# Kernel tuning notes

Measured on AMD Instinct MI355X. Metric: run time of the kernel, lower is better.

Reference implementation:

```python
import jax, jax.numpy as jnp
import numpy as np

E, H, I, T, K = 32, 1024, 768, 2048, 8


def setup_inputs() -> dict:
    key = jax.random.key(0)
    ks = jax.random.split(key, 6)
    hidden_states = jax.random.normal(ks[0], (T, H), dtype=jnp.float32)
    routing_weights = jax.random.uniform(ks[1], (T, K), dtype=jnp.float32)
    selected_experts = jax.random.randint(ks[2], (T, K), 0, E, dtype=jnp.int32)
    scale = 0.02
    gate_proj = jax.random.normal(ks[3], (E, I, H), dtype=jnp.float32) * scale
    up_proj = jax.random.normal(ks[4], (E, I, H), dtype=jnp.float32) * scale
    down_proj = jax.random.normal(ks[5], (E, H, I), dtype=jnp.float32) * scale
    return {
        "hidden_states": hidden_states,
        "routing_weights": routing_weights,
        "selected_experts": selected_experts,
        "gate_proj": gate_proj,
        "up_proj": up_proj,
        "down_proj": down_proj,
    }


def reference(hidden_states, routing_weights, selected_experts, gate_proj, up_proj, down_proj):
    # hidden_states: [T, H]; routing_weights/selected_experts: [T, K]
    # gate/up: [E, I, H]; down: [E, H, I]
    T_, _ = hidden_states.shape
    E_ = gate_proj.shape[0]
    # combine[t, e] = sum_k routing_weights[t, k] * 1[selected_experts[t, k] == e]
    combine = jnp.zeros((T_, E_), hidden_states.dtype).at[
        jnp.arange(T_)[:, None], selected_experts
    ].add(routing_weights)
    g = jnp.einsum('th,eih->eti', hidden_states, gate_proj)   # [E, T, I]
    u = jnp.einsum('th,eih->eti', hidden_states, up_proj)     # [E, T, I]
    h = jax.nn.silu(g) * u                                    # SwiGLU
    d = jnp.einsum('eti,ehi->eth', h, down_proj)              # [E, T, H]
    out = jnp.einsum('eth,te->th', d, combine)                # weighted combine
    return out
```

## Files before the change

kernel.cpp:

```cpp
#include <hip/hip_runtime.h>
#include <hip/hip_bf16.h>
#include <math.h>

#define E_N 32
#define H_N 1024
#define I_N 768
#define T_N 2048
#define K_N 8
#define MT  128
#define NPAIRS (T_N * K_N)
#define MAX_SLOTS (NPAIRS + E_N * MT)
#define MAX_TILES (NPAIRS / MT + E_N)
#define RS 40

typedef __attribute__((ext_vector_type(8))) short bf16x8;
typedef __attribute__((ext_vector_type(4))) short bf16x4;
typedef __attribute__((ext_vector_type(8))) float f32x8;
typedef __attribute__((ext_vector_type(4))) float f32x4;

__device__ __forceinline__ unsigned pk2(float a, float b) {
    unsigned ua = __float_as_uint(a) + 0x8000u;
    unsigned ub = __float_as_uint(b) + 0x8000u;
    return (ua >> 16) | (ub & 0xffff0000u);
}
__device__ __forceinline__ bf16x8 cvt8(f32x8 v) {
    union { unsigned u[4]; bf16x8 h; } r;
    r.u[0] = pk2(v[0], v[1]); r.u[1] = pk2(v[2], v[3]);
    r.u[2] = pk2(v[4], v[5]); r.u[3] = pk2(v[6], v[7]);
    return r.h;
}
__device__ __forceinline__ float bf2f(short s) {
    return __uint_as_float(((unsigned)(unsigned short)s) << 16);
}

__global__ void route_kernel(const int* __restrict__ sel,
                             int* __restrict__ slot_token,
                             int* __restrict__ pair_slot,
                             int* __restrict__ tile_expert,
                             int* __restrict__ tile_row0,
                             int* __restrict__ n_tiles_out) {
    __shared__ int cnt[E_N], off[E_N], cur[E_N];
    int tid = threadIdx.x;
    if (tid < E_N) cnt[tid] = 0;
    __syncthreads();
    for (int p = tid; p < NPAIRS; p += blockDim.x)
        atomicAdd(&cnt[sel[p]], 1);
    __syncthreads();
    if (tid == 0) {
        int acc = 0, tt = 0;
        for (int e = 0; e < E_N; ++e) {
            off[e] = acc;
            cur[e] = 0;
            int nt = (cnt[e] + MT - 1) / MT;
            for (int i = 0; i < nt; ++i) {
                tile_expert[tt] = e;
                tile_row0[tt] = acc + i * MT;
                ++tt;
            }
            acc += nt * MT;
        }
        *n_tiles_out = tt;
    }
    __syncthreads();
    for (int p = tid; p < NPAIRS; p += blockDim.x) {
        int e = sel[p];
        int slot = off[e] + atomicAdd(&cur[e], 1);
        slot_token[slot] = p / K_N;
        pair_slot[p] = slot;
    }
}

__global__ __launch_bounds__(256) void gather_kernel(
    const float* __restrict__ hs,
    const int* __restrict__ slot_token,
    short* __restrict__ x_buf) {
    int idx = blockIdx.x * 256 + threadIdx.x;
    int slot = idx >> 8;
    int pos = (idx & 255) * 4;
    int tok = slot_token[slot];
    union { unsigned u[2]; bf16x4 s; } o;
    if (tok >= 0) {
        f32x4 v = *(const f32x4*)(hs + (size_t)tok * H_N + pos);
        o.u[0] = pk2(v[0], v[1]);
        o.u[1] = pk2(v[2], v[3]);
    } else {
        o.u[0] = 0; o.u[1] = 0;
    }
    *(bf16x4*)(x_buf + (size_t)slot * H_N + pos) = o.s;
}

__global__ __launch_bounds__(256, 2) void gateup_kernel(
    const short* __restrict__ x_buf,
    const float* __restrict__ gate,
    const float* __restrict__ up,
    const int* __restrict__ tile_expert,
    const int* __restrict__ tile_row0,
    const int* __restrict__ n_tiles,
    __hip_bfloat16* __restrict__ h_buf) {
    int id = blockIdx.x;
    int W = (id & 7) * 120 + (id >> 3);
    int tile = W % MAX_TILES;
    int ycol = W / MAX_TILES;
    if (tile >= *n_tiles) return;
    __shared__ short sA[128 * RS];
    __shared__ short sG[128 * RS];
    __shared__ short sU[128 * RS];
    int e = tile_expert[tile];
    int row0 = tile_row0[tile];
    int col0 = ycol * 128;
    int tid = threadIdx.x;
    int wave = tid >> 6, lane = tid & 63, quad = lane >> 4, r16 = lane & 15;
    int m0w = (wave >> 1) * 64, n0w = (wave & 1) * 64;
    int srow = tid >> 2;
    int scol = (tid & 3) * 8;

    f32x4 accG[4][4], accU[4][4];
#pragma unroll
    for (int i = 0; i < 4; ++i)
#pragma unroll
        for (int j = 0; j < 4; ++j) {
            accG[i][j] = (f32x4){0.f, 0.f, 0.f, 0.f};
            accU[i][j] = (f32x4){0.f, 0.f, 0.f, 0.f};
        }

    const size_t gbase = ((size_t)e * I_N + col0) * H_N;

    bf16x8 pa[2];
    f32x8 pg[2], pu[2];
#pragma unroll
    for (int r = 0; r < 2; ++r) {
        int row = r * 64 + srow;
        pa[r] = *(const bf16x8*)(x_buf + (size_t)(row0 + row) * H_N + scol);
        pg[r] = *(const f32x8*)(gate + gbase + (size_t)row * H_N + scol);
        pu[r] = *(const f32x8*)(up + gbase + (size_t)row * H_N + scol);
    }

#pragma unroll 1
    for (int k0 = 0; k0 < H_N; k0 += 32) {
        __syncthreads();
#pragma unroll
        for (int r = 0; r < 2; ++r) {
            int row = r * 64 + srow;
            *(bf16x8*)&sA[row * RS + scol] = pa[r];
            *(bf16x8*)&sG[row * RS + scol] = cvt8(pg[r]);
            *(bf16x8*)&sU[row * RS + scol] = cvt8(pu[r]);
        }
        __syncthreads();
        if (k0 + 32 < H_N) {
            int kn = k0 + 32;
#pragma unroll
            for (int r = 0; r < 2; ++r) {
                int row = r * 64 + srow;
                pa[r] = *(const bf16x8*)(x_buf + (size_t)(row0 + row) * H_N + kn + scol);
                pg[r] = *(const f32x8*)(gate + gbase + (size_t)row * H_N + kn + scol);
                pu[r] = *(const f32x8*)(up + gbase + (size_t)row * H_N + kn + scol);
            }
        }
        bf16x8 af[4], bg[4], bu[4];
#pragma unroll
        for (int mi = 0; mi < 4; ++mi)
            af[mi] = *(const bf16x8*)&sA[(m0w + mi * 16 + r16) * RS + quad * 8];
#pragma unroll
        for (int ni = 0; ni < 4; ++ni) {
            bg[ni] = *(const bf16x8*)&sG[(n0w + ni * 16 + r16) * RS + quad * 8];
            bu[ni] = *(const bf16x8*)&sU[(n0w + ni * 16 + r16) * RS + quad * 8];
        }
#pragma unroll
        for (int mi = 0; mi < 4; ++mi)
#pragma unroll
            for (int ni = 0; ni < 4; ++ni) {
                accG[mi][ni] = __builtin_amdgcn_mfma_f32_16x16x32_bf16(af[mi], bg[ni], accG[mi][ni], 0, 0, 0);
                accU[mi][ni] = __builtin_amdgcn_mfma_f32_16x16x32_bf16(af[mi], bu[ni], accU[mi][ni], 0, 0, 0);
            }
    }
#pragma unroll
    for (int mi = 0; mi < 4; ++mi)
#pragma unroll
        for (int ni = 0; ni < 4; ++ni)
#pragma unroll
            for (int r = 0; r < 4; ++r) {
                int m = m0w + mi * 16 + quad * 4 + r;
                int n = col0 + n0w + ni * 16 + r16;
                float g = accG[mi][ni][r], u = accU[mi][ni][r];
                float hval = g * u / (1.0f + __expf(-g));
                h_buf[(size_t)(row0 + m) * I_N + n] = __float2bfloat16(hval);
            }
}

__global__ __launch_bounds__(256, 2) void down_kernel(
    const __hip_bfloat16* __restrict__ h_buf,
    const float* __restrict__ down,
    const int* __restrict__ tile_expert,
    const int* __restrict__ tile_row0,
    const int* __restrict__ n_tiles,
    short* __restrict__ d_buf) {
    int id = blockIdx.x;
    int W = (id & 7) * 160 + (id >> 3);
    int tile = W % MAX_TILES;
    int ycol = W / MAX_TILES;
    if (tile >= *n_tiles) return;
    __shared__ short sA[128 * RS];
    __shared__ short sB[128 * RS];
    int e = tile_expert[tile];
    int row0 = tile_row0[tile];
    int col0 = ycol * 128;
    int tid = threadIdx.x;
    int wave = tid >> 6, lane = tid & 63, quad = lane >> 4, r16 = lane & 15;
    int m0w = (wave >> 1) * 64, n0w = (wave & 1) * 64;
    int srow = tid >> 2;
    int scol = (tid & 3) * 8;

    f32x4 acc[4][4];
#pragma unroll
    for (int i = 0; i < 4; ++i)
#pragma unroll
        for (int j = 0; j < 4; ++j) acc[i][j] = (f32x4){0.f, 0.f, 0.f, 0.f};

    const short* hb = (const short*)h_buf;
    const size_t dbase = ((size_t)e * H_N + col0) * I_N;

    bf16x8 pa[2];
    f32x8 pb[2];
#pragma unroll
    for (int r = 0; r < 2; ++r) {
        int row = r * 64 + srow;
        pa[r] = *(const bf16x8*)(hb + (size_t)(row0 + row) * I_N + scol);
        pb[r] = *(const f32x8*)(down + dbase + (size_t)row * I_N + scol);
    }

#pragma unroll 1
    for (int k0 = 0; k0 < I_N; k0 += 32) {
        __syncthreads();
#pragma unroll
        for (int r = 0; r < 2; ++r) {
            int row = r * 64 + srow;
            *(bf16x8*)&sA[row * RS + scol] = pa[r];
            *(bf16x8*)&sB[row * RS + scol] = cvt8(pb[r]);
        }
        __syncthreads();
        if (k0 + 32 < I_N) {
            int kn = k0 + 32;
#pragma unroll
            for (int r = 0; r < 2; ++r) {
                int row = r * 64 + srow;
                pa[r] = *(const bf16x8*)(hb + (size_t)(row0 + row) * I_N + kn + scol);
                pb[r] = *(const f32x8*)(down + dbase + (size_t)row * I_N + kn + scol);
            }
        }
        bf16x8 af[4], bf[4];
#pragma unroll
        for (int mi = 0; mi < 4; ++mi)
            af[mi] = *(const bf16x8*)&sA[(m0w + mi * 16 + r16) * RS + quad * 8];
#pragma unroll
        for (int ni = 0; ni < 4; ++ni)
            bf[ni] = *(const bf16x8*)&sB[(n0w + ni * 16 + r16) * RS + quad * 8];
#pragma unroll
        for (int mi = 0; mi < 4; ++mi)
#pragma unroll
            for (int ni = 0; ni < 4; ++ni)
                acc[mi][ni] = __builtin_amdgcn_mfma_f32_16x16x32_bf16(af[mi], bf[ni], acc[mi][ni], 0, 0, 0);
    }
#pragma unroll
    for (int mi = 0; mi < 4; ++mi)
#pragma unroll
        for (int ni = 0; ni < 4; ++ni)
#pragma unroll
            for (int r = 0; r < 4; ++r) {
                int m = m0w + mi * 16 + quad * 4 + r;
                int n = col0 + n0w + ni * 16 + r16;
                unsigned u = __float_as_uint(acc[mi][ni][r]) + 0x8000u;
                d_buf[(size_t)(row0 + m) * H_N + n] = (short)(u >> 16);
            }
}

__global__ __launch_bounds__(256) void combine_kernel(
    const short* __restrict__ d_buf,
    const int* __restrict__ pair_slot,
    const float* __restrict__ rw,
    float* __restrict__ out) {
    int idx = blockIdx.x * blockDim.x + threadIdx.x;
    int t = idx >> 10;
    int h = idx & (H_N - 1);
    float acc = 0.f;
#pragma unroll
    for (int k = 0; k < K_N; ++k) {
        int slot = pair_slot[t * K_N + k];
        float w = rw[t * K_N + k];
        acc += w * bf2f(d_buf[(size_t)slot * H_N + h]);
    }
    out[idx] = acc;
}

extern "C" void kernel_launch(void* const* d_in, const int* in_sizes, int n_in,
                              void* d_out, int out_size, void* d_ws, size_t ws_size,
                              hipStream_t stream) {
    const float* hs   = (const float*)d_in[0];
    const float* rw   = (const float*)d_in[1];
    const int*   sel  = (const int*)d_in[2];
    const float* gate = (const float*)d_in[3];
    const float* up   = (const float*)d_in[4];
    const float* down = (const float*)d_in[5];
    float* out = (float*)d_out;

    char* ws = (char*)d_ws;
    int* slot_token  = (int*)ws;  ws += ((size_t)MAX_SLOTS * 4 + 255) / 256 * 256;
    int* pair_slot   = (int*)ws;  ws += ((size_t)NPAIRS * 4 + 255) / 256 * 256;
    int* tile_expert = (int*)ws;  ws += ((size_t)MAX_TILES * 4 + 255) / 256 * 256;
    int* tile_row0   = (int*)ws;  ws += ((size_t)MAX_TILES * 4 + 255) / 256 * 256;
    int* n_tiles     = (int*)ws;  ws += 256;
    short* x_buf = (short*)ws;    ws += ((size_t)MAX_SLOTS * H_N * 2 + 255) / 256 * 256;
    __hip_bfloat16* h_buf = (__hip_bfloat16*)ws;
    short* d_buf = x_buf;

    hipMemsetAsync(slot_token, 0xFF, (size_t)MAX_SLOTS * 4, stream);
    route_kernel<<<1, 256, 0, stream>>>(sel, slot_token, pair_slot,
                                        tile_expert, tile_row0, n_tiles);
    gather_kernel<<<(MAX_SLOTS * H_N / 4) / 256, 256, 0, stream>>>(hs, slot_token, x_buf);

    gateup_kernel<<<MAX_TILES * (I_N / 128), 256, 0, stream>>>(
        x_buf, gate, up, tile_expert, tile_row0, n_tiles, h_buf);

    down_kernel<<<MAX_TILES * (H_N / 128), 256, 0, stream>>>(
        h_buf, down, tile_expert, tile_row0, n_tiles, d_buf);

    combine_kernel<<<(T_N * H_N) / 256, 256, 0, stream>>>(d_buf, pair_slot,
                                                          rw, out);
}
```

Baseline: 490.3 us.

## Double-buffer LDS tiles in gate/up and down GEMMs with one barrier per step

Both grouped GEMM kernels now keep two LDS buffers. Each iteration reads fragments from the current buffer, writes the prefetched next tile into the other buffer, issues global loads two steps ahead, and ends with a single barrier instead of two. MFMA blocks are wrapped in s_setprio, and the LDS row stride changes from 40 to 36 shorts to alter bank mapping. This doubles LDS use, which may limit occupancy. The new padding may also misalign the 16-byte vector LDS accesses or raise bank conflicts.

Measured after the change: 486.5 us. No clear change (-0.8%).

```diff
diff --git a/kernel.cpp b/kernel.cpp
--- a/kernel.cpp
+++ b/kernel.cpp
@@ -11,7 +11,7 @@
 #define NPAIRS (T_N * K_N)
 #define MAX_SLOTS (NPAIRS + E_N * MT)
 #define MAX_TILES (NPAIRS / MT + E_N)
-#define RS 40
+#define RS 36
 
 typedef __attribute__((ext_vector_type(8))) short bf16x8;
 typedef __attribute__((ext_vector_type(4))) short bf16x4;
@@ -31,6 +31,11 @@
 }
 __device__ __forceinline__ float bf2f(short s) {
     return __uint_as_float(((unsigned)(unsigned short)s) << 16);
+}
+
+__device__ __forceinline__ void lds_barrier() {
+    asm volatile("s_waitcnt lgkmcnt(0)" ::: "memory");
+    __builtin_amdgcn_s_barrier();
 }
 
 __global__ void route_kernel(const int* __restrict__ sel,
@@ -102,9 +107,9 @@
     int tile = W % MAX_TILES;
     int ycol = W / MAX_TILES;
     if (tile >= *n_tiles) return;
-    __shared__ short sA[128 * RS];
-    __shared__ short sG[128 * RS];
-    __shared__ short sU[128 * RS];
+    __shared__ short sA[2][128 * RS];
+    __shared__ short sG[2][128 * RS];
+    __shared__ short sU[2][128 * RS];
     int e = tile_expert[tile];
     int row0 = tile_row0[tile];
     int col0 = ycol * 128;
@@ -124,47 +129,66 @@
         }
 
     const size_t gbase = ((size_t)e * I_N + col0) * H_N;
+    const short* xrow = x_buf + (size_t)row0 * H_N;
 
     bf16x8 pa[2];
     f32x8 pg[2], pu[2];
 #pragma unroll
     for (int r = 0; r < 2; ++r) {
         int row = r * 64 + srow;
-        pa[r] = *(const bf16x8*)(x_buf + (size_t)(row0 + row) * H_N + scol);
+        pa[r] = *(const bf16x8*)(xrow + (size_t)row * H_N + scol);
         pg[r] = *(const f32x8*)(gate + gbase + (size_t)row * H_N + scol);
         pu[r] = *(const f32x8*)(up + gbase + (size_t)row * H_N + scol);
     }
-
+#pragma unroll
+    for (int r = 0; r < 2; ++r) {
+        int row = r * 64 + srow;
+        *(bf16x8*)&sA[0][row * RS + scol] = pa[r];
+        *(bf16x8*)&sG[0][row * RS + scol] = cvt8(pg[r]);
+        *(bf16x8*)&sU[0][row * RS + scol] = cvt8(pu[r]);
+    }
+#pragma unroll
+    for (int r = 0; r < 2; ++r) {
+        int row = r * 64 + srow;
+        pa[r] = *(const bf16x8*)(xrow + (size_t)row * H_N + 32 + scol);
+        pg[r] = *(const f32x8*)(gate + gbase + (size_t)row * H_N + 32 + scol);
+        pu[r] = *(const f32x8*)(up + gbase + (size_t)row * H_N + 32 + scol);
+    }
+    lds_barrier();
+
+    int cur = 0;
 #pragma unroll 1
     for (int k0 = 0; k0 < H_N; k0 += 32) {
-        __syncthreads();
-#pragma unroll
-        for (int r = 0; r < 2; ++r) {
-            int row = r * 64 + srow;
-            *(bf16x8*)&sA[row * RS + scol] = pa[r];
-            *(bf16x8*)&sG[row * RS + scol] = cvt8(pg[r]);
-            *(bf16x8*)&sU[row * RS + scol] = cvt8(pu[r]);
-        }
-        __syncthreads();
+        bf16x8 af[4], bg[4], bu[4];
+#pragma unroll
+        for (int mi = 0; mi < 4; ++mi)
+            af[mi] = *(const bf16x8*)&sA[cur][(m0w + mi * 16 + r16) * RS + quad * 8];
+#pragma unroll
+        for (int ni = 0; ni < 4; ++ni) {
+            bg[ni] = *(const bf16x8*)&sG[cur][(n0w + ni * 16 + r16) * RS + quad * 8];
+            bu[ni] = *(const bf16x8*)&sU[cur][(n0w + ni * 16 + r16) * RS + quad * 8];
+        }
         if (k0 + 32 < H_N) {
-            int kn = k0 + 32;
+            int nxt = cur ^ 1;
 #pragma unroll
             for (int r = 0; r < 2; ++r) {
                 int row = r * 64 + srow;
-                pa[r] = *(const bf16x8*)(x_buf + (size_t)(row0 + row) * H_N + kn + scol);
-                pg[r] = *(const f32x8*)(gate + gbase + (size_t)row * H_N + kn + scol);
-                pu[r] = *(const f32x8*)(up + gbase + (size_t)row * H_N + kn + scol);
-            }
-        }
-        bf16x8 af[4], bg[4], bu[4];
-#pragma unroll
-        for (int mi = 0; mi < 4; ++mi)
-            af[mi] = *(const bf16x8*)&sA[(m0w + mi * 16 + r16) * RS + quad * 8];
-#pragma unroll
-        for (int ni = 0; ni < 4; ++ni) {
-            bg[ni] = *(const bf16x8*)&sG[(n0w + ni * 16 + r16) * RS + quad * 8];
-            bu[ni] = *(const bf16x8*)&sU[(n0w + ni * 16 + r16) * RS + quad * 8];
-        }
+                *(bf16x8*)&sA[nxt][row * RS + scol] = pa[r];
+                *(bf16x8*)&sG[nxt][row * RS + scol] = cvt8(pg[r]);
+                *(bf16x8*)&sU[nxt][row * RS + scol] = cvt8(pu[r]);
+            }
+            if (k0 + 64 < H_N) {
+                int kn = k0 + 64;
+#pragma unroll
+                for (int r = 0; r < 2; ++r) {
+                    int row = r * 64 + srow;
+                    pa[r] = *(const bf16x8*)(xrow + (size_t)row * H_N + kn + scol);
+                    pg[r] = *(const f32x8*)(gate + gbase + (size_t)row * H_N + kn + scol);
+                    pu[r] = *(const f32x8*)(up + gbase + (size_t)row * H_N + kn + scol);
+                }
+            }
+        }
+        __builtin_amdgcn_s_setprio(1);
 #pragma unroll
         for (int mi = 0; mi < 4; ++mi)
 #pragma unroll
@@ -172,6 +196,9 @@
                 accG[mi][ni] = __builtin_amdgcn_mfma_f32_16x16x32_bf16(af[mi], bg[ni], accG[mi][ni], 0, 0, 0);
                 accU[mi][ni] = __builtin_amdgcn_mfma_f32_16x16x32_bf16(af[mi], bu[ni], accU[mi][ni], 0, 0, 0);
             }
+        __builtin_amdgcn_s_setprio(0);
+        if (k0 + 32 < H_N) lds_barrier();
+        cur ^= 1;
     }
 #pragma unroll
     for (int mi = 0; mi < 4; ++mi)
@@ -199,8 +226,8 @@
     int tile = W % MAX_TILES;
     int ycol = W / MAX_TILES;
     if (tile >= *n_tiles) return;
-    __shared__ short sA[128 * RS];
-    __shared__ short sB[128 * RS];
+    __shared__ short sA[2][128 * RS];
+    __shared__ short sB[2][128 * RS];
     int e = tile_expert[tile];
     int row0 = tile_row0[tile];
     int col0 = ycol * 128;
@@ -218,47 +245,67 @@
 
     const short* hb = (const short*)h_buf;
     const size_t dbase = ((size_t)e * H_N + col0) * I_N;
+    const short* hrow = hb + (size_t)row0 * I_N;
 
     bf16x8 pa[2];
     f32x8 pb[2];
 #pragma unroll
     for (int r = 0; r < 2; ++r) {
         int row = r * 64 + srow;
-        pa[r] = *(const bf16x8*)(hb + (size_t)(row0 + row) * I_N + scol);
+        pa[r] = *(const bf16x8*)(hrow + (size_t)row * I_N + scol);
         pb[r] = *(const f32x8*)(down + dbase + (size_t)row * I_N + scol);
     }
-
+#pragma unroll
+    for (int r = 0; r < 2; ++r) {
+        int row = r * 64 + srow;
+        *(bf16x8*)&sA[0][row * RS + scol] = pa[r];
+        *(bf16x8*)&sB[0][row * RS + scol] = cvt8(pb[r]);
+    }
+#pragma unroll
+    for (int r = 0; r < 2; ++r) {
+        int row = r * 64 + srow;
+        pa[r] = *(const bf16x8*)(hrow + (size_t)row * I_N + 32 + scol);
+        pb[r] = *(const f32x8*)(down + dbase + (size_t)row * I_N + 32 + scol);
+    }
+    lds_barrier();
+
+    int cur = 0;
 #pragma unroll 1
     for (int k0 = 0; k0 < I_N; k0 += 32) {
-        __syncthreads();
-#pragma unroll
-        for (int r = 0; r < 2; ++r) {
-            int row = r * 64 + srow;
-            *(bf16x8*)&sA[row * RS + scol] = pa[r];
-            *(bf16x8*)&sB[row * RS + scol] = cvt8(pb[r]);
-        }
-        __syncthreads();
+        bf16x8 af[4], bf[4];
+#pragma unroll
+        for (int mi = 0; mi < 4; ++mi)
+            af[mi] = *(const bf16x8*)&sA[cur][(m0w + mi * 16 + r16) * RS + quad * 8];
+#pragma unroll
+        for (int ni = 0; ni < 4; ++ni)
+            bf[ni] = *(const bf16x8*)&sB[cur][(n0w + ni * 16 + r16) * RS + quad * 8];
         if (k0 + 32 < I_N) {
-            int kn = k0 + 32;
+            int nxt = cur ^ 1;
 #pragma unroll
             for (int r = 0; r < 2; ++r) {
                 int row = r * 64 + srow;
-                pa[r] = *(const bf16x8*)(hb + (size_t)(row0 + row) * I_N + kn + scol);
-                pb[r] = *(const f32x8*)(down + dbase + (size_t)row * I_N + kn + scol);
-            }
-        }
-        bf16x8 af[4], bf[4];
-#pragma unroll
-        for (int mi = 0; mi < 4; ++mi)
-            af[mi] = *(const bf16x8*)&sA[(m0w + mi * 16 + r16) * RS + quad * 8];
-#pragma unroll
-        for (int ni = 0; ni < 4; ++ni)
-            bf[ni] = *(const bf16x8*)&sB[(n0w + ni * 16 + r16) * RS + quad * 8];
+                *(bf16x8*)&sA[nxt][row * RS + scol] = pa[r];
+                *(bf16x8*)&sB[nxt][row * RS + scol] = cvt8(pb[r]);
+            }
+            if (k0 + 64 < I_N) {
+                int kn = k0 + 64;
+#pragma unroll
+                for (int r = 0; r < 2; ++r) {
+                    int row = r * 64 + srow;
+                    pa[r] = *(const bf16x8*)(hrow + (size_t)row * I_N + kn + scol);
+                    pb[r] = *(const f32x8*)(down + dbase + (size_t)row * I_N + kn + scol);
+                }
+            }
+        }
+        __builtin_amdgcn_s_setprio(1);
 #pragma unroll
         for (int mi = 0; mi < 4; ++mi)
 #pragma unroll
             for (int ni = 0; ni < 4; ++ni)
                 acc[mi][ni] = __builtin_amdgcn_mfma_f32_16x16x32_bf16(af[mi], bf[ni], acc[mi][ni], 0, 0, 0);
+        __builtin_amdgcn_s_setprio(0);
+        if (k0 + 32 < I_N) lds_barrier();
+        cur ^= 1;
     }
 #pragma unroll
     for (int mi = 0; mi < 4; ++mi)
```

## Pre-convert expert weights to bf16 and stage tiles via direct global-to-LDS loads

Applied to the files above, without the earlier changes.

Adds a conversion pass that writes the gate, up and down weights to bf16 in workspace, so the GEMM kernels read half as many bytes per tile and skip the per-tile fp32-to-bf16 conversion. The GEMM tile loads now use global_load_lds to write straight into unpadded LDS, replacing the register prefetch double-buffer. MFMA sections are wrapped in s_setprio, and down_kernel's launch bound rises to 3 blocks. The trade-offs: the weights are fully read and rewritten on every call, the overlap from register prefetch is lost, and the unpadded LDS layout may cause bank conflicts.

Result: slower. 524.2 us (+6.9%).

```diff
diff --git a/kernel.cpp b/kernel.cpp
--- a/kernel.cpp
+++ b/kernel.cpp
@@ -11,7 +11,6 @@
 #define NPAIRS (T_N * K_N)
 #define MAX_SLOTS (NPAIRS + E_N * MT)
 #define MAX_TILES (NPAIRS / MT + E_N)
-#define RS 40
 
 typedef __attribute__((ext_vector_type(8))) short bf16x8;
 typedef __attribute__((ext_vector_type(4))) short bf16x4;
@@ -31,6 +30,12 @@
 }
 __device__ __forceinline__ float bf2f(short s) {
     return __uint_as_float(((unsigned)(unsigned short)s) << 16);
+}
+
+__device__ __forceinline__ void gload16(const void* g, void* l) {
+    __builtin_amdgcn_global_load_lds(
+        (const __attribute__((address_space(1))) unsigned int*)g,
+        (__attribute__((address_space(3))) unsigned int*)l, 16, 0, 0);
 }
 
 __global__ void route_kernel(const int* __restrict__ sel,
@@ -89,10 +94,20 @@
     *(bf16x4*)(x_buf + (size_t)slot * H_N + pos) = o.s;
 }
 
+__global__ __launch_bounds__(256) void cvt_kernel(
+    const float* __restrict__ src, short* __restrict__ dst, int n8) {
+    int i = blockIdx.x * 256 + threadIdx.x;
+    int stride = gridDim.x * 256;
+    for (; i < n8; i += stride) {
+        f32x8 v = *(const f32x8*)(src + (size_t)i * 8);
+        *(bf16x8*)(dst + (size_t)i * 8) = cvt8(v);
+    }
+}
+
 __global__ __launch_bounds__(256, 2) void gateup_kernel(
     const short* __restrict__ x_buf,
-    const float* __restrict__ gate,
-    const float* __restrict__ up,
+    const short* __restrict__ wg,
+    const short* __restrict__ wu,
     const int* __restrict__ tile_expert,
     const int* __restrict__ tile_row0,
     const int* __restrict__ n_tiles,
@@ -102,17 +117,17 @@
     int tile = W % MAX_TILES;
     int ycol = W / MAX_TILES;
     if (tile >= *n_tiles) return;
-    __shared__ short sA[128 * RS];
-    __shared__ short sG[128 * RS];
-    __shared__ short sU[128 * RS];
+    __shared__ short sA[128 * 32];
+    __shared__ short sG[128 * 32];
+    __shared__ short sU[128 * 32];
     int e = tile_expert[tile];
     int row0 = tile_row0[tile];
     int col0 = ycol * 128;
     int tid = threadIdx.x;
     int wave = tid >> 6, lane = tid & 63, quad = lane >> 4, r16 = lane & 15;
     int m0w = (wave >> 1) * 64, n0w = (wave & 1) * 64;
-    int srow = tid >> 2;
-    int scol = (tid & 3) * 8;
+    int srow = lane >> 2;
+    int scb = (lane & 3) * 8;
 
     f32x4 accG[4][4], accU[4][4];
 #pragma unroll
@@ -123,48 +138,32 @@
             accU[i][j] = (f32x4){0.f, 0.f, 0.f, 0.f};
         }
 
-    const size_t gbase = ((size_t)e * I_N + col0) * H_N;
-
-    bf16x8 pa[2];
-    f32x8 pg[2], pu[2];
-#pragma unroll
-    for (int r = 0; r < 2; ++r) {
-        int row = r * 64 + srow;
-        pa[r] = *(const bf16x8*)(x_buf + (size_t)(row0 + row) * H_N + scol);
-        pg[r] = *(const f32x8*)(gate + gbase + (size_t)row * H_N + scol);
-        pu[r] = *(const f32x8*)(up + gbase + (size_t)row * H_N + scol);
-    }
+    const short* Ag = x_buf + (size_t)row0 * H_N;
+    const short* Gg = wg + ((size_t)e * I_N + col0) * H_N;
+    const short* Ug = wu + ((size_t)e * I_N + col0) * H_N;
 
 #pragma unroll 1
     for (int k0 = 0; k0 < H_N; k0 += 32) {
         __syncthreads();
 #pragma unroll
-        for (int r = 0; r < 2; ++r) {
-            int row = r * 64 + srow;
-            *(bf16x8*)&sA[row * RS + scol] = pa[r];
-            *(bf16x8*)&sG[row * RS + scol] = cvt8(pg[r]);
-            *(bf16x8*)&sU[row * RS + scol] = cvt8(pu[r]);
+        for (int c = 0; c < 2; ++c) {
+            int rb = (wave * 2 + c) * 16;
+            size_t goff = (size_t)(rb + srow) * H_N + k0 + scb;
+            gload16(Ag + goff, &sA[rb * 32]);
+            gload16(Gg + goff, &sG[rb * 32]);
+            gload16(Ug + goff, &sU[rb * 32]);
         }
         __syncthreads();
-        if (k0 + 32 < H_N) {
-            int kn = k0 + 32;
-#pragma unroll
-            for (int r = 0; r < 2; ++r) {
-                int row = r * 64 + srow;
-                pa[r] = *(const bf16x8*)(x_buf + (size_t)(row0 + row) * H_N + kn + scol);
-                pg[r] = *(const f32x8*)(gate + gbase + (size_t)row * H_N + kn + scol);
-                pu[r] = *(const f32x8*)(up + gbase + (size_t)row * H_N + kn + scol);
-            }
-        }
         bf16x8 af[4], bg[4], bu[4];
 #pragma unroll
         for (int mi = 0; mi < 4; ++mi)
-            af[mi] = *(const bf16x8*)&sA[(m0w + mi * 16 + r16) * RS + quad * 8];
+            af[mi] = *(const bf16x8*)&sA[(m0w + mi * 16 + r16) * 32 + quad * 8];
 #pragma unroll
         for (int ni = 0; ni < 4; ++ni) {
-            bg[ni] = *(const bf16x8*)&sG[(n0w + ni * 16 + r16) * RS + quad * 8];
-            bu[ni] = *(const bf16x8*)&sU[(n0w + ni * 16 + r16) * RS + quad * 8];
-        }
+            bg[ni] = *(const bf16x8*)&sG[(n0w + ni * 16 + r16) * 32 + quad * 8];
+            bu[ni] = *(const bf16x8*)&sU[(n0w + ni * 16 + r16) * 32 + quad * 8];
+        }
+        __builtin_amdgcn_s_setprio(1);
 #pragma unroll
         for (int mi = 0; mi < 4; ++mi)
 #pragma unroll
@@ -172,6 +171,7 @@
                 accG[mi][ni] = __builtin_amdgcn_mfma_f32_16x16x32_bf16(af[mi], bg[ni], accG[mi][ni], 0, 0, 0);
                 accU[mi][ni] = __builtin_amdgcn_mfma_f32_16x16x32_bf16(af[mi], bu[ni], accU[mi][ni], 0, 0, 0);
             }
+        __builtin_amdgcn_s_setprio(0);
     }
 #pragma unroll
     for (int mi = 0; mi < 4; ++mi)
@@ -187,9 +187,9 @@
             }
 }
 
-__global__ __launch_bounds__(256, 2) void down_kernel(
+__global__ __launch_bounds__(256, 3) void down_kernel(
     const __hip_bfloat16* __restrict__ h_buf,
-    const float* __restrict__ down,
+    const short* __restrict__ wd,
     const int* __restrict__ tile_expert,
     const int* __restrict__ tile_row0,
     const int* __restrict__ n_tiles,
@@ -199,16 +199,16 @@
     int tile = W % MAX_TILES;
     int ycol = W / MAX_TILES;
     if (tile >= *n_tiles) return;
-    __shared__ short sA[128 * RS];
-    __shared__ short sB[128 * RS];
+    __shared__ short sA[128 * 32];
+    __shared__ short sB[128 * 32];
     int e = tile_expert[tile];
     int row0 = tile_row0[tile];
     int col0 = ycol * 128;
     int tid = threadIdx.x;
     int wave = tid >> 6, lane = tid & 63, quad = lane >> 4, r16 = lane & 15;
     int m0w = (wave >> 1) * 64, n0w = (wave & 1) * 64;
-    int srow = tid >> 2;
-    int scol = (tid & 3) * 8;
+    int srow = lane >> 2;
+    int scb = (lane & 3) * 8;
 
     f32x4 acc[4][4];
 #pragma unroll
@@ -216,49 +216,34 @@
 #pragma unroll
         for (int j = 0; j < 4; ++j) acc[i][j] = (f32x4){0.f, 0.f, 0.f, 0.f};
 
-    const short* hb = (const short*)h_buf;
-    const size_t dbase = ((size_t)e * H_N + col0) * I_N;
-
-    bf16x8 pa[2];
-    f32x8 pb[2];
-#pragma unroll
-    for (int r = 0; r < 2; ++r) {
-        int row = r * 64 + srow;
-        pa[r] = *(const bf16x8*)(hb + (size_t)(row0 + row) * I_N + scol);
-        pb[r] = *(const f32x8*)(down + dbase + (size_t)row * I_N + scol);
-    }
+    const short* Ag = (const short*)h_buf + (size_t)row0 * I_N;
+    const short* Bg = wd + ((size_t)e * H_N + col0) * I_N;
 
 #pragma unroll 1
     for (int k0 = 0; k0 < I_N; k0 += 32) {
         __syncthreads();
 #pragma unroll
-        for (int r = 0; r < 2; ++r) {
-            int row = r * 64 + srow;
-            *(bf16x8*)&sA[row * RS + scol] = pa[r];
-            *(bf16x8*)&sB[row * RS + scol] = cvt8(pb[r]);
+        for (int c = 0; c < 2; ++c) {
+            int rb = (wave * 2 + c) * 16;
+            size_t goff = (size_t)(rb + srow) * I_N + k0 + scb;
+            gload16(Ag + goff, &sA[rb * 32]);
+            gload16(Bg + goff, &sB[rb * 32]);
         }
         __syncthreads();
-        if (k0 + 32 < I_N) {
-            int kn = k0 + 32;
-#pragma unroll
-            for (int r = 0; r < 2; ++r) {
-                int row = r * 64 + srow;
-                pa[r] = *(const bf16x8*)(hb + (size_t)(row0 + row) * I_N + kn + scol);
-                pb[r] = *(const f32x8*)(down + dbase + (size_t)row * I_N + kn + scol);
-            }
-        }
         bf16x8 af[4], bf[4];
 #pragma unroll
         for (int mi = 0; mi < 4; ++mi)
-            af[mi] = *(const bf16x8*)&sA[(m0w + mi * 16 + r16) * RS + quad * 8];
+            af[mi] = *(const bf16x8*)&sA[(m0w + mi * 16 + r16) * 32 + quad * 8];
 #pragma unroll
         for (int ni = 0; ni < 4; ++ni)
-            bf[ni] = *(const bf16x8*)&sB[(n0w + ni * 16 + r16) * RS + quad * 8];
+            bf[ni] = *(const bf16x8*)&sB[(n0w + ni * 16 + r16) * 32 + quad * 8];
+        __builtin_amdgcn_s_setprio(1);
 #pragma unroll
         for (int mi = 0; mi < 4; ++mi)
 #pragma unroll
             for (int ni = 0; ni < 4; ++ni)
                 acc[mi][ni] = __builtin_amdgcn_mfma_f32_16x16x32_bf16(af[mi], bf[ni], acc[mi][ni], 0, 0, 0);
+        __builtin_amdgcn_s_setprio(0);
     }
 #pragma unroll
     for (int mi = 0; mi < 4; ++mi)
@@ -302,6 +287,7 @@
     const float* down = (const float*)d_in[5];
     float* out = (float*)d_out;
 
+    const size_t WN = (size_t)E_N * I_N * H_N;
     char* ws = (char*)d_ws;
     int* slot_token  = (int*)ws;  ws += ((size_t)MAX_SLOTS * 4 + 255) / 256 * 256;
     int* pair_slot   = (int*)ws;  ws += ((size_t)NPAIRS * 4 + 255) / 256 * 256;
@@ -310,6 +296,10 @@
     int* n_tiles     = (int*)ws;  ws += 256;
     short* x_buf = (short*)ws;    ws += ((size_t)MAX_SLOTS * H_N * 2 + 255) / 256 * 256;
     __hip_bfloat16* h_buf = (__hip_bfloat16*)ws;
+    ws += ((size_t)MAX_SLOTS * I_N * 2 + 255) / 256 * 256;
+    short* wg = (short*)ws;
+    short* wu = wg + WN;
+    short* wd = wg;
     short* d_buf = x_buf;
 
     hipMemsetAsync(slot_token, 0xFF, (size_t)MAX_SLOTS * 4, stream);
@@ -317,11 +307,17 @@
                                         tile_expert, tile_row0, n_tiles);
     gather_kernel<<<(MAX_SLOTS * H_N / 4) / 256, 256, 0, stream>>>(hs, slot_token, x_buf);
 
+    const int N8 = (int)(WN / 8);
+    cvt_kernel<<<2048, 256, 0, stream>>>(gate, wg, N8);
+    cvt_kernel<<<2048, 256, 0, stream>>>(up, wu, N8);
+
     gateup_kernel<<<MAX_TILES * (I_N / 128), 256, 0, stream>>>(
-        x_buf, gate, up, tile_expert, tile_row0, n_tiles, h_buf);
+        x_buf, wg, wu, tile_expert, tile_row0, n_tiles, h_buf);
+
+    cvt_kernel<<<2048, 256, 0, stream>>>(down, wd, N8);
 
     down_kernel<<<MAX_TILES * (H_N / 128), 256, 0, stream>>>(
-        h_buf, down, tile_expert, tile_row0, n_tiles, d_buf);
+        h_buf, wd, tile_expert, tile_row0, n_tiles, d_buf);
 
     combine_kernel<<<(T_N * H_N) / 256, 256, 0, stream>>>(d_buf, pair_slot,
                                                           rw, out);
```
